# Kernel optimization log

Hardware: AMD Instinct MI355X
Metric: run time of the kernel (lower is better)

The kernel has to match this reference:

```python
import jax, jax.numpy as jnp
from jax import lax
import numpy as np

B, L, E, H = 4, 512, 1024, 128


def setup_inputs() -> dict:
    key = jax.random.key(0)
    k0, k1, k2, k3, k4, k5 = jax.random.split(key, 6)
    s = 1.0 / np.sqrt(E)
    return {
        "rec_emb": jax.random.normal(k0, (B, L, E), jnp.float32),
        "lig_emb": jax.random.normal(k1, (B, L, E), jnp.float32),
        "W1": jax.random.normal(k2, (E, H), jnp.float32) * s,
        "b1": jax.random.normal(k3, (H,), jnp.float32) * 0.01,
        "conv_w": jax.random.normal(k4, (1, H, 2, 2), jnp.float32) * (1.0 / np.sqrt(H * 4)),
        "conv_b": jax.random.normal(k5, (1,), jnp.float32) * 0.01,
    }


def reference(rec_emb, lig_emb, W1, b1, conv_w, conv_b):
    # shared fc: Linear -> ReLU (Dropout is identity in eval mode)
    rec_hid = jax.nn.relu(jnp.einsum("bie,eh->bih", rec_emb, W1) + b1)
    lig_hid = jax.nn.relu(jnp.einsum("bje,eh->bjh", lig_emb, W1) + b1)
    # outer-product bilinear map: bih,bjh->bijh, then tanh
    mat = jnp.tanh(rec_hid[:, :, None, :] * lig_hid[:, None, :, :])
    # permute to NCHW: (b, h, i, j)
    mat = jnp.transpose(mat, (0, 3, 1, 2))
    # Conv2d(H -> 1, kernel=2, padding=1): out spatial = L + 1
    y = lax.conv_general_dilated(
        mat, conv_w, window_strides=(1, 1), padding=[(1, 1), (1, 1)],
        dimension_numbers=("NCHW", "OIHW", "NCHW"),
    ) + conv_b[None, :, None, None]
    # MaxPool2d(kernel=2, stride=2), floor mode
    pooled = lax.reduce_window(
        y, -jnp.inf, lax.max,
        window_dimensions=(1, 1, 2, 2), window_strides=(1, 1, 2, 2),
        padding="VALID",
    )
    # global max over spatial dims -> (b, 1), sigmoid, flatten
    m = jnp.max(pooled, axis=(2, 3))
    return jax.nn.sigmoid(m).reshape(-1)
```

## Files before the change

### kernel.cpp

```cpp
#include <hip/hip_runtime.h>
#include <hip/hip_fp16.h>
#include <math.h>

#define BDIM 4
#define LDIM 512
#define EDIM 1024
#define HDIM 128
#define TILE 31
#define NT   17
#define K2   2.885390081777927f

typedef unsigned short ushort_t;
typedef __attribute__((ext_vector_type(8))) _Float16 half8;
typedef __attribute__((ext_vector_type(4))) float f32x4;

struct __align__(16) H8 { __half2 p[4]; };
union HU { H8 h; half8 v; };

__global__ __launch_bounds__(256) void wcvt(const float* __restrict__ W1,
                                            ushort_t* __restrict__ Wt) {
  const int g = (int)blockIdx.x * 256 + threadIdx.x;
  const int n = g & 127, k8 = g >> 7;
  float v[8];
#pragma unroll
  for (int j = 0; j < 8; ++j) v[j] = W1[(size_t)(k8 * 8 + j) * HDIM + n];
  H8 o;
#pragma unroll
  for (int j = 0; j < 4; ++j) o.p[j] = __floats2half2_rn(v[2 * j], v[2 * j + 1]);
  *(H8*)&Wt[(size_t)n * EDIM + k8 * 8] = o;
}

__global__ __launch_bounds__(256) void gemm_direct(
    const float* __restrict__ rec, const float* __restrict__ lig,
    const ushort_t* __restrict__ Wt, const float* __restrict__ b1,
    ushort_t* __restrict__ hid) {
  const int gw = (int)blockIdx.x * 4 + (threadIdx.x >> 6);
  const int l = threadIdx.x & 63;
  const int strip = gw >> 3;
  const int nidx = gw & 7;
  const int r0 = strip * 16;
  const int m = l & 15, q = l >> 4;
  const float* arow = ((r0 < BDIM * LDIM)
                           ? rec + (size_t)r0 * EDIM
                           : lig + (size_t)(r0 - BDIM * LDIM) * EDIM) +
                      (size_t)m * EDIM + q * 8;
  const ushort_t* brow = Wt + (size_t)(nidx * 16 + m) * EDIM + q * 8;

  f32x4 acc = {0.f, 0.f, 0.f, 0.f};
  for (int blk = 0; blk < 8; ++blk) {
    float4 alo[4], ahi[4];
    half8 bf[4];
#pragma unroll
    for (int j = 0; j < 4; ++j) {
      const int k0 = (blk * 4 + j) * 32;
      alo[j] = *(const float4*)(arow + k0);
      ahi[j] = *(const float4*)(arow + k0 + 4);
      bf[j] = *(const half8*)(brow + k0);
    }
#pragma unroll
    for (int j = 0; j < 4; ++j) {
      HU au;
      au.h.p[0] = __floats2half2_rn(alo[j].x, alo[j].y);
      au.h.p[1] = __floats2half2_rn(alo[j].z, alo[j].w);
      au.h.p[2] = __floats2half2_rn(ahi[j].x, ahi[j].y);
      au.h.p[3] = __floats2half2_rn(ahi[j].z, ahi[j].w);
      acc = __builtin_amdgcn_mfma_f32_16x16x32_f16(au.v, bf[j], acc, 0, 0, 0);
    }
  }

  const float scale = (r0 < BDIM * LDIM) ? -K2 : 1.0f;
  const int col = nidx * 16 + m;
  const float bias = b1[col];
#pragma unroll
  for (int r = 0; r < 4; ++r) {
    float v = fmaxf(acc[r] + bias, 0.f) * scale;
    ((_Float16*)hid)[(size_t)(r0 + q * 4 + r) * HDIM + col] = (_Float16)v;
  }
}

__global__ __launch_bounds__(256, 4) void bilinear_max(
    const ushort_t* __restrict__ hid, const float* __restrict__ cw,
    const float* __restrict__ cb, float* __restrict__ partial) {
  __shared__ ushort_t rl[32][136];
  __shared__ ushort_t ll[32][136];
  __shared__ float4 sl[32][33];
  __shared__ float wred[4];
  __shared__ float wpart[2][4];

  const int t = threadIdx.x;
  const int b = blockIdx.z;
  const int ib = (int)blockIdx.y * TILE - 1;
  const int jb = (int)blockIdx.x * TILE - 1;
  const int w = t >> 6, l = t & 63;
  const int q = l >> 4, c15 = l & 15;

  if (t < HDIM) {
    float4 w4 = *(const float4*)&cw[t * 4];
#pragma unroll
    for (int off = 32; off > 0; off >>= 1) {
      w4.x += __shfl_down(w4.x, off, 64);
      w4.y += __shfl_down(w4.y, off, 64);
      w4.z += __shfl_down(w4.z, off, 64);
      w4.w += __shfl_down(w4.w, off, 64);
    }
    if ((t & 63) == 0) {
      wpart[t >> 6][0] = w4.x; wpart[t >> 6][1] = w4.y;
      wpart[t >> 6][2] = w4.z; wpart[t >> 6][3] = w4.w;
    }
  }

  half8 wf[4];
#pragma unroll
  for (int c = 0; c < 4; ++c) {
#pragma unroll
    for (int j = 0; j < 8; ++j) {
      float v = (c15 < 4) ? cw[(size_t)(c * 32 + q * 8 + j) * 4 + c15] : 0.f;
      wf[c][j] = (_Float16)(-2.f * v);
    }
  }

  H8 z;
  z.p[0] = z.p[1] = z.p[2] = z.p[3] = __floats2half2_rn(0.f, 0.f);
  for (int p = t; p < 1024; p += 256) {
    int r = p >> 4, seg = (p & 15) * 8;
    if (r < 32) {
      int i = ib + r;
      H8 v = z;
      if (i >= 0 && i < LDIM) v = *(const H8*)&hid[((size_t)(b * LDIM + i)) * HDIM + seg];
      *(H8*)&rl[r][seg] = v;
    } else {
      int j = jb + (r - 32);
      H8 v = z;
      if (j >= 0 && j < LDIM) v = *(const H8*)&hid[((size_t)((BDIM + b) * LDIM + j)) * HDIM + seg];
      *(H8*)&ll[r - 32][seg] = v;
    }
  }
  __syncthreads();
  const float wsum_v = (c15 < 4) ? (wpart[0][c15] + wpart[1][c15]) : 0.f;

  const __half2 D0 = __float2half2_rn(0.998539f);
  const __half2 D1 = __float2half2_rn(-0.947090f);
  const __half2 D2 = __float2half2_rn(0.676154f);
  const __half2 D3 = __float2half2_rn(-0.228646f);

#define POLYG(U) \
  __hmul2(U, __hfma2(U, __hfma2(U, __hfma2(U, D3, D2), D1), D0))

  for (int g = 0; g < 16; ++g) {
    const int ii = w * 8 + (g >> 1);
    const int jj0 = (g & 1) << 4;
    f32x4 acc = {0.f, 0.f, 0.f, 0.f};
#pragma unroll
    for (int c = 0; c < 4; ++c) {
      HU ru, lu, gu;
      ru.v = *(const half8*)&rl[ii][c * 32 + q * 8];
      lu.v = *(const half8*)&ll[jj0 + c15][c * 32 + q * 8];
      __half2 u0 = h2exp2(__hmul2(ru.h.p[0], lu.h.p[0]));
      __half2 u1 = h2exp2(__hmul2(ru.h.p[1], lu.h.p[1]));
      __half2 u2 = h2exp2(__hmul2(ru.h.p[2], lu.h.p[2]));
      __half2 u3 = h2exp2(__hmul2(ru.h.p[3], lu.h.p[3]));
      gu.h.p[0] = POLYG(u0);
      gu.h.p[1] = POLYG(u1);
      gu.h.p[2] = POLYG(u2);
      gu.h.p[3] = POLYG(u3);
      acc = __builtin_amdgcn_mfma_f32_16x16x32_f16(gu.v, wf[c], acc, 0, 0, 0);
    }
    if (c15 < 4) {
#pragma unroll
      for (int r = 0; r < 4; ++r)
        ((float*)&sl[ii][jj0 + q * 4 + r])[c15] = wsum_v + acc[r];
    }
  }
#undef POLYG
  __syncthreads();

  float m = -INFINITY;
  const float cbv = cb[0];
  for (int p = t; p < 1024; p += 256) {
    int jj = p & 31, iy = p >> 5;
    int i = ib + iy, j = jb + jj;
    if (iy > 0 && jj > 0 && i < LDIM && j < LDIM) {
      float v = cbv + sl[iy - 1][jj - 1].x + sl[iy - 1][jj].y
                    + sl[iy][jj - 1].z + sl[iy][jj].w;
      m = fmaxf(m, v);
    }
  }
#pragma unroll
  for (int off = 32; off > 0; off >>= 1) m = fmaxf(m, __shfl_down(m, off, 64));
  if ((t & 63) == 0) wred[t >> 6] = m;
  __syncthreads();
  if (t == 0) {
    float mm = fmaxf(fmaxf(wred[0], wred[1]), fmaxf(wred[2], wred[3]));
    partial[((size_t)b * NT + blockIdx.y) * NT + blockIdx.x] = mm;
  }
}

__global__ __launch_bounds__(64) void finalize(const float* __restrict__ partial,
                                               float* __restrict__ out) {
  const int b = blockIdx.x, t = threadIdx.x;
  float m = -INFINITY;
  for (int p = t; p < NT * NT; p += 64) m = fmaxf(m, partial[b * NT * NT + p]);
#pragma unroll
  for (int off = 32; off > 0; off >>= 1) m = fmaxf(m, __shfl_down(m, off, 64));
  if (t == 0) out[b] = 1.f / (1.f + expf(-m));
}

extern "C" void kernel_launch(void* const* d_in, const int* in_sizes, int n_in,
                              void* d_out, int out_size, void* d_ws, size_t ws_size,
                              hipStream_t stream) {
  const float* rec = (const float*)d_in[0];
  const float* lig = (const float*)d_in[1];
  const float* W1  = (const float*)d_in[2];
  const float* b1  = (const float*)d_in[3];
  const float* cw  = (const float*)d_in[4];
  const float* cb  = (const float*)d_in[5];
  float* out = (float*)d_out;

  ushort_t* Wt   = (ushort_t*)d_ws;
  ushort_t* hid  = Wt + (size_t)HDIM * EDIM;
  float* partial = (float*)(hid + (size_t)2 * BDIM * LDIM * HDIM);

  wcvt<<<dim3(64), 256, 0, stream>>>(W1, Wt);
  gemm_direct<<<dim3(512), 256, 0, stream>>>(rec, lig, Wt, b1, hid);
  bilinear_max<<<dim3(NT, NT, BDIM), 256, 0, stream>>>(hid, cw, cb, partial);
  finalize<<<dim3(BDIM), 64, 0, stream>>>(partial, out);
}
```

Measured before the change: 131.3 us.

## Use power-of-two 32x32 tiles with a scalar-computed halo row and column

Changes the bilinear tile from 31 to 32 output positions, so the grid shrinks from 17x17 to 16x16 blocks per batch and the store-side bounds checks go away. The extra halo row and column (65 entries) that the conv needs is computed after the MFMA loop by a scalar per-thread loop over all 128 hidden channels. The aim is fewer, better aligned blocks and less duplicated halo work. The cost is a serial tail that runs on only about one wave while the others wait. The new 130-element LDS row stride also breaks 16-byte alignment for the half8 loads and stores.

```diff
diff --git a/kernel.cpp b/kernel.cpp
--- a/kernel.cpp
+++ b/kernel.cpp
@@ -6,8 +6,8 @@
 #define LDIM 512
 #define EDIM 1024
 #define HDIM 128
-#define TILE 31
-#define NT   17
+#define TILE 32
+#define NT   16
 #define K2   2.885390081777927f
 
 typedef unsigned short ushort_t;
@@ -67,7 +67,6 @@
       acc = __builtin_amdgcn_mfma_f32_16x16x32_f16(au.v, bf[j], acc, 0, 0, 0);
     }
   }
-
   const float scale = (r0 < BDIM * LDIM) ? -K2 : 1.0f;
   const int col = nidx * 16 + m;
   const float bias = b1[col];
@@ -81,9 +80,9 @@
 __global__ __launch_bounds__(256, 4) void bilinear_max(
     const ushort_t* __restrict__ hid, const float* __restrict__ cw,
     const float* __restrict__ cb, float* __restrict__ partial) {
-  __shared__ ushort_t rl[32][136];
-  __shared__ ushort_t ll[32][136];
-  __shared__ float4 sl[32][33];
+  __shared__ ushort_t rl[33][130];
+  __shared__ ushort_t ll[33][130];
+  __shared__ float4 sl[33][34];
   __shared__ float wred[4];
   __shared__ float wpart[2][4];
 
@@ -121,18 +120,18 @@
 
   H8 z;
   z.p[0] = z.p[1] = z.p[2] = z.p[3] = __floats2half2_rn(0.f, 0.f);
-  for (int p = t; p < 1024; p += 256) {
+  for (int p = t; p < 66 * 16; p += 256) {
     int r = p >> 4, seg = (p & 15) * 8;
-    if (r < 32) {
+    if (r < 33) {
       int i = ib + r;
       H8 v = z;
-      if (i >= 0 && i < LDIM) v = *(const H8*)&hid[((size_t)(b * LDIM + i)) * HDIM + seg];
+      if (i >= 0) v = *(const H8*)&hid[((size_t)(b * LDIM + i)) * HDIM + seg];
       *(H8*)&rl[r][seg] = v;
     } else {
-      int j = jb + (r - 32);
+      int j = jb + (r - 33);
       H8 v = z;
-      if (j >= 0 && j < LDIM) v = *(const H8*)&hid[((size_t)((BDIM + b) * LDIM + j)) * HDIM + seg];
-      *(H8*)&ll[r - 32][seg] = v;
+      if (j >= 0) v = *(const H8*)&hid[((size_t)((BDIM + b) * LDIM + j)) * HDIM + seg];
+      *(H8*)&ll[r - 33][seg] = v;
     }
   }
   __syncthreads();
@@ -142,7 +141,6 @@
   const __half2 D1 = __float2half2_rn(-0.947090f);
   const __half2 D2 = __float2half2_rn(0.676154f);
   const __half2 D3 = __float2half2_rn(-0.228646f);
-
 #define POLYG(U) \
   __hmul2(U, __hfma2(U, __hfma2(U, __hfma2(U, D3, D2), D1), D0))
 
@@ -172,18 +170,37 @@
     }
   }
 #undef POLYG
+
+  if (t < 65) {
+    const int pi = (t < 33) ? t : 32;
+    const int qj = (t < 33) ? 32 : (t - 33);
+    const float ws0 = wpart[0][0] + wpart[1][0];
+    const float ws1 = wpart[0][1] + wpart[1][1];
+    const float ws2 = wpart[0][2] + wpart[1][2];
+    const float ws3 = wpart[0][3] + wpart[1][3];
+    float4 sa = make_float4(0.f, 0.f, 0.f, 0.f);
+    for (int h = 0; h < HDIM; ++h) {
+      float rv = (float)(*(const _Float16*)&rl[pi][h]);
+      float lv = (float)(*(const _Float16*)&ll[qj][h]);
+      float u = __builtin_amdgcn_exp2f(rv * lv);
+      float gg = u * fmaf(u, fmaf(u, fmaf(u, -0.228646f, 0.676154f), -0.947090f), 0.998539f);
+      float4 w4 = *(const float4*)&cw[h * 4];
+      sa.x = fmaf(-2.f * gg, w4.x, sa.x);
+      sa.y = fmaf(-2.f * gg, w4.y, sa.y);
+      sa.z = fmaf(-2.f * gg, w4.z, sa.z);
+      sa.w = fmaf(-2.f * gg, w4.w, sa.w);
+    }
+    sl[pi][qj] = make_float4(ws0 + sa.x, ws1 + sa.y, ws2 + sa.z, ws3 + sa.w);
+  }
   __syncthreads();
 
   float m = -INFINITY;
   const float cbv = cb[0];
   for (int p = t; p < 1024; p += 256) {
-    int jj = p & 31, iy = p >> 5;
-    int i = ib + iy, j = jb + jj;
-    if (iy > 0 && jj > 0 && i < LDIM && j < LDIM) {
-      float v = cbv + sl[iy - 1][jj - 1].x + sl[iy - 1][jj].y
-                    + sl[iy][jj - 1].z + sl[iy][jj].w;
-      m = fmaxf(m, v);
-    }
+    int jj = (p & 31) + 1, iy = (p >> 5) + 1;
+    float v = cbv + sl[iy - 1][jj - 1].x + sl[iy - 1][jj].y
+                  + sl[iy][jj - 1].z + sl[iy][jj].w;
+    m = fmaxf(m, v);
   }
 #pragma unroll
   for (int off = 32; off > 0; off >>= 1) m = fmaxf(m, __shfl_down(m, off, 64));
```

Result: no change. 132.7 us (+1.0%).
